# Optimization experiments

Measured on AMD Instinct MI355X. Metric: run time of the kernel, lower is better.

## Reference

```python
import jax, jax.numpy as jnp
import numpy as np

EPS = 1e-8  # torch F.cosine_similarity default eps


def setup_inputs() -> dict:
    key = jax.random.key(0)
    k1, k2 = jax.random.split(key)
    xs_pad = jax.random.normal(k1, (8, 4096, 512), dtype=jnp.float32)
    spk_emb = jax.random.normal(k2, (8, 256, 512), dtype=jnp.float32)
    return {"xs_pad": xs_pad, "spk_emb": spk_emb}


def reference(xs_pad, spk_emb):
    # Faithful to F.cosine_similarity(x.unsqueeze(2), y.unsqueeze(1), dim=-1):
    #   dot(x, y) / (max(||x||, eps) * max(||y||, eps))
    # Implemented as L2-normalize then a batched GEMM -> (B, T, S), avoiding
    # the (B, T, S, D) broadcast intermediate.
    x_norm = jnp.maximum(jnp.linalg.norm(xs_pad, axis=-1, keepdims=True), EPS)
    y_norm = jnp.maximum(jnp.linalg.norm(spk_emb, axis=-1, keepdims=True), EPS)
    xn = xs_pad / x_norm          # (B, T, D)
    yn = spk_emb / y_norm         # (B, S, D)
    scores = jnp.einsum('btd,bsd->bts', xn, yn)  # (B, T, S)
    return scores
```

## Files before the change

kernel.cpp:

```cpp
#include <hip/hip_runtime.h>
#include <hip/hip_bf16.h>

#define BB 8
#define TT 4096
#define SS 256
#define DD 512

typedef __attribute__((ext_vector_type(8))) short short8;
typedef __attribute__((ext_vector_type(4))) float floatx4;
typedef __attribute__((ext_vector_type(4))) int intx4;

__device__ inline int pk2(float a, float b) {
  __hip_bfloat162 h = __float22bfloat162_rn(make_float2(a, b));
  int r;
  __builtin_memcpy(&r, &h, 4);
  return r;
}

__device__ inline short8 cvt8(float4 f0, float4 f1) {
  intx4 p;
  p[0] = pk2(f0.x, f0.y);
  p[1] = pk2(f0.z, f0.w);
  p[2] = pk2(f1.x, f1.y);
  p[3] = pk2(f1.z, f1.w);
  return __builtin_bit_cast(short8, p);
}

__global__ __launch_bounds__(256) void cos_packB_kernel(
    const float* __restrict__ spk, short* __restrict__ bp) {
  const int id = blockIdx.x;
  const int ks = id & 1;
  const int kt = (id >> 1) & 7;
  const int wn = (id >> 4) & 1;
  const int tn = (id >> 5) & 1;
  const int b = id >> 6;
  const int t = threadIdx.x;
  const int in = t >> 6;
  const int lane = t & 63;
  const int row = tn * 128 + wn * 64 + in * 16 + (lane & 15);
  const int k = kt * 64 + ks * 32 + (lane >> 4) * 8;
  const float* src = spk + ((size_t)(b * SS + row)) * DD + k;
  float4 f0 = *(const float4*)src;
  float4 f1 = *(const float4*)(src + 4);
  short8 o = cvt8(f0, f1);
  size_t frag = (size_t)((((b * 2 + tn) * 2 + wn) * 8 + kt) * 2 + ks) * 4 + in;
  *(short8*)(bp + frag * 512 + (size_t)lane * 8) = o;
}

__global__ __launch_bounds__(256) void cos_fused_kernel(
    const float* __restrict__ xs, const short* __restrict__ bp,
    float* __restrict__ out) {
  __shared__ float sA[2 * 128 * 64];
  float* scX = sA;
  float* scY = sA + 128;

  const int tid = threadIdx.x;
  const int wave = tid >> 6;
  const int lane = tid & 63;

  const int id = blockIdx.x;
  const int xcd = id & 7;
  const int j = id >> 3;
  const int pairIdx = xcd * 32 + (j >> 1);
  const int tn = j & 1;
  const int tm = pairIdx & 31;
  const int b = pairIdx >> 5;

  const int wm = wave >> 1;
  const int wn = wave & 1;
  const int quad = lane >> 4;
  const int l15 = lane & 15;
  const bool gramA = (wm == wn);

  const float* Abase = xs + ((size_t)b * TT + tm * 128) * DD;
  const short* Bw =
      bp + (size_t)((b * 2 + tn) * 2 + wn) * 32768 + (size_t)lane * 8;

  floatx4 acc[4][4];
#pragma unroll
  for (int i = 0; i < 4; i++)
#pragma unroll
    for (int jj = 0; jj < 4; jj++) acc[i][jj] = (floatx4){0.f, 0.f, 0.f, 0.f};
  floatx4 accG[4];
#pragma unroll
  for (int i = 0; i < 4; i++) accG[i] = (floatx4){0.f, 0.f, 0.f, 0.f};

  int aoff[8];
#pragma unroll
  for (int jj = 0; jj < 8; jj++) {
    int s = jj * 256 + tid;
    int row = s >> 4;
    int blk = (s & 15) ^ (row & 15);
    aoff[jj] = row * DD + blk * 4;
  }

#pragma unroll
  for (int jj = 0; jj < 8; jj++) {
    __builtin_amdgcn_global_load_lds(
        (const __attribute__((address_space(1))) unsigned int*)(Abase +
            aoff[jj]),
        (__attribute__((address_space(3))) unsigned int*)(sA +
            (jj * 256 + wave * 64) * 4),
        16, 0, 0);
  }
  __syncthreads();

  for (int kt = 0; kt < 8; ++kt) {
    const int cur = kt & 1;

    short8 breg[2][4];
    const short* Bkt = Bw + kt * 4096;
#pragma unroll
    for (int ksl = 0; ksl < 2; ksl++)
#pragma unroll
      for (int in = 0; in < 4; in++)
        breg[ksl][in] = *(const short8*)(Bkt + ksl * 2048 + in * 512);

    if (kt < 7) {
#pragma unroll
      for (int jj = 0; jj < 8; jj++) {
        __builtin_amdgcn_global_load_lds(
            (const __attribute__((address_space(1))) unsigned int*)(Abase +
                aoff[jj] + (kt + 1) * 64),
            (__attribute__((address_space(3))) unsigned int*)(sA +
                (cur ^ 1) * 8192 + (jj * 256 + wave * 64) * 4),
            16, 0, 0);
      }
    }

    const float* sAc = sA + cur * 8192;
#pragma unroll
    for (int ks = 0; ks < 2; ks++) {
      short8 af[4];
      const int b0s = ks * 8 + quad * 2;
#pragma unroll
      for (int im = 0; im < 4; im++) {
        int row = wm * 64 + im * 16 + l15;
        int s0 = b0s ^ (row & 15);
        int s1 = (b0s + 1) ^ (row & 15);
        float4 f0 = *(const float4*)(sAc + row * 64 + s0 * 4);
        float4 f1 = *(const float4*)(sAc + row * 64 + s1 * 4);
        af[im] = cvt8(f0, f1);
      }
#pragma unroll
      for (int im = 0; im < 4; im++)
#pragma unroll
        for (int in = 0; in < 4; in++)
          acc[im][in] = __builtin_amdgcn_mfma_f32_16x16x32_bf16(
              af[im], breg[ks][in], acc[im][in], 0, 0, 0);
      if (gramA) {
#pragma unroll
        for (int im = 0; im < 4; im++)
          accG[im] = __builtin_amdgcn_mfma_f32_16x16x32_bf16(
              af[im], af[im], accG[im], 0, 0, 0);
      } else {
#pragma unroll
        for (int in = 0; in < 4; in++)
          accG[in] = __builtin_amdgcn_mfma_f32_16x16x32_bf16(
              breg[ks][in], breg[ks][in], accG[in], 0, 0, 0);
      }
    }
    __syncthreads();
  }

  if (quad == (l15 >> 2)) {
#pragma unroll
    for (int i = 0; i < 4; i++) {
      float inv = 1.0f / fmaxf(sqrtf(accG[i][l15 & 3]), 1e-8f);
      if (gramA)
        scX[wm * 64 + i * 16 + l15] = inv;
      else
        scY[wn * 64 + i * 16 + l15] = inv;
    }
  }
  __syncthreads();

  float* Obase = out + ((size_t)b * TT + tm * 128) * SS + tn * 128;
#pragma unroll
  for (int im = 0; im < 4; im++) {
#pragma unroll
    for (int in = 0; in < 4; in++) {
      int col = wn * 64 + in * 16 + l15;
      float yv = scY[col];
#pragma unroll
      for (int r = 0; r < 4; r++) {
        int row = wm * 64 + im * 16 + quad * 4 + r;
        Obase[row * SS + col] = acc[im][in][r] * scX[row] * yv;
      }
    }
  }
}

extern "C" void kernel_launch(void* const* d_in, const int* in_sizes, int n_in,
                              void* d_out, int out_size, void* d_ws,
                              size_t ws_size, hipStream_t stream) {
  const float* xs = (const float*)d_in[0];
  const float* spk = (const float*)d_in[1];
  float* out = (float*)d_out;
  short* bp = (short*)d_ws;

  hipLaunchKernelGGL(cos_packB_kernel, dim3(512), dim3(256), 0, stream, spk,
                     bp);
  hipLaunchKernelGGL(cos_fused_kernel, dim3(512), dim3(256), 0, stream, xs,
                     bp, out);
}
```

Baseline: 117.6 us.

## Deepen A-tile pipeline to four stages with half-width K slices and prefetched B

Replaces the two-buffer 64-wide K staging of the fp32 A tile with a four-buffer ring of 32-wide slices, keeping three tiles of global-to-LDS loads in flight. Explicit vmcnt waits and raw s_barrier replace the full __syncthreads, and B fragments are register-prefetched one step ahead. Launch bounds now request two blocks per CU. The aim is to hide global load latency behind MFMA work; in exchange the hand-tuned vmcnt counts are fragile, and the register cap may cause spills.

```diff
diff --git a/kernel.cpp b/kernel.cpp
--- a/kernel.cpp
+++ b/kernel.cpp
@@ -47,10 +47,10 @@
   *(short8*)(bp + frag * 512 + (size_t)lane * 8) = o;
 }
 
-__global__ __launch_bounds__(256) void cos_fused_kernel(
+__global__ __launch_bounds__(256, 2) void cos_fused_kernel(
     const float* __restrict__ xs, const short* __restrict__ bp,
     float* __restrict__ out) {
-  __shared__ float sA[2 * 128 * 64];
+  __shared__ float sA[4 * 128 * 32];
   float* scX = sA;
   float* scY = sA + 128;
 
@@ -85,83 +85,97 @@
 #pragma unroll
   for (int i = 0; i < 4; i++) accG[i] = (floatx4){0.f, 0.f, 0.f, 0.f};
 
-  int aoff[8];
-#pragma unroll
-  for (int jj = 0; jj < 8; jj++) {
+  int aoff[4];
+#pragma unroll
+  for (int jj = 0; jj < 4; jj++) {
     int s = jj * 256 + tid;
-    int row = s >> 4;
-    int blk = (s & 15) ^ (row & 15);
+    int row = s >> 3;
+    int blk = (s & 7) ^ (row & 7);
     aoff[jj] = row * DD + blk * 4;
   }
 
-#pragma unroll
-  for (int jj = 0; jj < 8; jj++) {
-    __builtin_amdgcn_global_load_lds(
-        (const __attribute__((address_space(1))) unsigned int*)(Abase +
-            aoff[jj]),
-        (__attribute__((address_space(3))) unsigned int*)(sA +
-            (jj * 256 + wave * 64) * 4),
-        16, 0, 0);
-  }
+#define STAGE(KT)                                                           \
+  do {                                                                      \
+    _Pragma("unroll") for (int jj = 0; jj < 4; jj++) {                      \
+      __builtin_amdgcn_global_load_lds(                                     \
+          (const __attribute__((address_space(1))) unsigned int*)(Abase +   \
+              aoff[jj] + (KT) * 32),                                        \
+          (__attribute__((address_space(3))) unsigned int*)(sA +            \
+              ((KT) & 3) * 4096 + (jj * 256 + wave * 64) * 4),              \
+          16, 0, 0);                                                        \
+    }                                                                       \
+  } while (0)
+
+  short8 breg[2][4];
+
+#pragma unroll
+  for (int in = 0; in < 4; in++)
+    breg[0][in] = *(const short8*)(Bw + in * 512);
+  STAGE(0);
+  __builtin_amdgcn_sched_barrier(0);
+  STAGE(1);
+  STAGE(2);
+  asm volatile("s_waitcnt vmcnt(8)" ::: "memory");
+  __builtin_amdgcn_sched_barrier(0);
+  __builtin_amdgcn_s_barrier();
+  __builtin_amdgcn_sched_barrier(0);
+
+#pragma unroll
+  for (int kt = 0; kt < 16; ++kt) {
+    if (kt + 1 < 16) {
+      const short* Bn = Bw + ((kt + 1) >> 1) * 4096 + ((kt + 1) & 1) * 2048;
+#pragma unroll
+      for (int in = 0; in < 4; in++)
+        breg[(kt + 1) & 1][in] = *(const short8*)(Bn + in * 512);
+    }
+    if (kt + 3 < 16) STAGE(kt + 3);
+
+    const float* sAc = sA + (kt & 3) * 4096;
+    short8 af[4];
+#pragma unroll
+    for (int im = 0; im < 4; im++) {
+      int row = wm * 64 + im * 16 + l15;
+      int r7 = l15 & 7;
+      int s0 = (quad * 2) ^ r7;
+      int s1 = (quad * 2 + 1) ^ r7;
+      float4 f0 = *(const float4*)(sAc + row * 32 + s0 * 4);
+      float4 f1 = *(const float4*)(sAc + row * 32 + s1 * 4);
+      af[im] = cvt8(f0, f1);
+    }
+#pragma unroll
+    for (int im = 0; im < 4; im++)
+#pragma unroll
+      for (int in = 0; in < 4; in++)
+        acc[im][in] = __builtin_amdgcn_mfma_f32_16x16x32_bf16(
+            af[im], breg[kt & 1][in], acc[im][in], 0, 0, 0);
+    if (gramA) {
+#pragma unroll
+      for (int im = 0; im < 4; im++)
+        accG[im] = __builtin_amdgcn_mfma_f32_16x16x32_bf16(
+            af[im], af[im], accG[im], 0, 0, 0);
+    } else {
+#pragma unroll
+      for (int in = 0; in < 4; in++)
+        accG[in] = __builtin_amdgcn_mfma_f32_16x16x32_bf16(
+            breg[kt & 1][in], breg[kt & 1][in], accG[in], 0, 0, 0);
+    }
+
+    if (kt < 15) {
+      if (kt == 0)
+        asm volatile("s_waitcnt vmcnt(12)" ::: "memory");
+      else if (kt <= 12)
+        asm volatile("s_waitcnt vmcnt(16)" ::: "memory");
+      else if (kt == 13)
+        asm volatile("s_waitcnt vmcnt(12)" ::: "memory");
+      else
+        asm volatile("s_waitcnt vmcnt(8)" ::: "memory");
+      __builtin_amdgcn_sched_barrier(0);
+      __builtin_amdgcn_s_barrier();
+      __builtin_amdgcn_sched_barrier(0);
+    }
+  }
+#undef STAGE
   __syncthreads();
-
-  for (int kt = 0; kt < 8; ++kt) {
-    const int cur = kt & 1;
-
-    short8 breg[2][4];
-    const short* Bkt = Bw + kt * 4096;
-#pragma unroll
-    for (int ksl = 0; ksl < 2; ksl++)
-#pragma unroll
-      for (int in = 0; in < 4; in++)
-        breg[ksl][in] = *(const short8*)(Bkt + ksl * 2048 + in * 512);
-
-    if (kt < 7) {
-#pragma unroll
-      for (int jj = 0; jj < 8; jj++) {
-        __builtin_amdgcn_global_load_lds(
-            (const __attribute__((address_space(1))) unsigned int*)(Abase +
-                aoff[jj] + (kt + 1) * 64),
-            (__attribute__((address_space(3))) unsigned int*)(sA +
-                (cur ^ 1) * 8192 + (jj * 256 + wave * 64) * 4),
-            16, 0, 0);
-      }
-    }
-
-    const float* sAc = sA + cur * 8192;
-#pragma unroll
-    for (int ks = 0; ks < 2; ks++) {
-      short8 af[4];
-      const int b0s = ks * 8 + quad * 2;
-#pragma unroll
-      for (int im = 0; im < 4; im++) {
-        int row = wm * 64 + im * 16 + l15;
-        int s0 = b0s ^ (row & 15);
-        int s1 = (b0s + 1) ^ (row & 15);
-        float4 f0 = *(const float4*)(sAc + row * 64 + s0 * 4);
-        float4 f1 = *(const float4*)(sAc + row * 64 + s1 * 4);
-        af[im] = cvt8(f0, f1);
-      }
-#pragma unroll
-      for (int im = 0; im < 4; im++)
-#pragma unroll
-        for (int in = 0; in < 4; in++)
-          acc[im][in] = __builtin_amdgcn_mfma_f32_16x16x32_bf16(
-              af[im], breg[ks][in], acc[im][in], 0, 0, 0);
-      if (gramA) {
-#pragma unroll
-        for (int im = 0; im < 4; im++)
-          accG[im] = __builtin_amdgcn_mfma_f32_16x16x32_bf16(
-              af[im], af[im], accG[im], 0, 0, 0);
-      } else {
-#pragma unroll
-        for (int in = 0; in < 4; in++)
-          accG[in] = __builtin_amdgcn_mfma_f32_16x16x32_bf16(
-              breg[ks][in], breg[ks][in], accG[in], 0, 0, 0);
-      }
-    }
-    __syncthreads();
-  }
 
   if (quad == (l15 >> 2)) {
 #pragma unroll
```

New measurement: 120.1 us. 1.02x slower.

## Load A fragments directly from global into registers with 3-stage prefetch

Applied to the files above, without the earlier changes.

Replaces the LDS-staged A tile (global_load_lds with double buffering and per-k-tile barriers) with direct per-lane global float4 loads into a triple-buffered register pipeline, prefetching two k-slices ahead together with B fragments. This removes LDS traffic and the __syncthreads in the main loop, and lowers LDS use so more blocks can be resident. In exchange, each wave pair with the same wm now loads its A rows separately, doubling A global/L2 traffic, and the register buffers raise VGPR pressure, which could lower occupancy.

```diff
diff --git a/kernel.cpp b/kernel.cpp
--- a/kernel.cpp
+++ b/kernel.cpp
@@ -50,9 +50,8 @@
 __global__ __launch_bounds__(256) void cos_fused_kernel(
     const float* __restrict__ xs, const short* __restrict__ bp,
     float* __restrict__ out) {
-  __shared__ float sA[2 * 128 * 64];
-  float* scX = sA;
-  float* scY = sA + 128;
+  __shared__ float scX[128];
+  __shared__ float scY[128];
 
   const int tid = threadIdx.x;
   const int wave = tid >> 6;
@@ -72,7 +71,13 @@
   const int l15 = lane & 15;
   const bool gramA = (wm == wn);
 
-  const float* Abase = xs + ((size_t)b * TT + tm * 128) * DD;
+  const float* Arow[4];
+#pragma unroll
+  for (int im = 0; im < 4; im++)
+    Arow[im] = xs +
+               ((size_t)b * TT + tm * 128 + wm * 64 + im * 16 + l15) * DD +
+               quad * 8;
+
   const short* Bw =
       bp + (size_t)((b * 2 + tn) * 2 + wn) * 32768 + (size_t)lane * 8;
 
@@ -85,83 +90,62 @@
 #pragma unroll
   for (int i = 0; i < 4; i++) accG[i] = (floatx4){0.f, 0.f, 0.f, 0.f};
 
-  int aoff[8];
-#pragma unroll
-  for (int jj = 0; jj < 8; jj++) {
-    int s = jj * 256 + tid;
-    int row = s >> 4;
-    int blk = (s & 15) ^ (row & 15);
-    aoff[jj] = row * DD + blk * 4;
-  }
+  float4 abuf[3][8];
+  short8 bbuf[3][4];
+
+#define LOADA(S)                                                        \
+  do {                                                                  \
+    _Pragma("unroll") for (int im_ = 0; im_ < 4; im_++) {               \
+      const float* p_ = Arow[im_] + ((S) >> 1) * 64 + ((S) & 1) * 32;   \
+      abuf[(S) % 3][im_ * 2] = *(const float4*)p_;                      \
+      abuf[(S) % 3][im_ * 2 + 1] = *(const float4*)(p_ + 4);            \
+    }                                                                   \
+  } while (0)
+
+#define LOADB(S)                                                        \
+  do {                                                                  \
+    const short* q_ = Bw + ((S) >> 1) * 4096 + ((S) & 1) * 2048;        \
+    _Pragma("unroll") for (int in_ = 0; in_ < 4; in_++)                 \
+      bbuf[(S) % 3][in_] = *(const short8*)(q_ + in_ * 512);            \
+  } while (0)
+
+  LOADA(0);
+  LOADB(0);
+  LOADA(1);
+  LOADB(1);
 
 #pragma unroll
-  for (int jj = 0; jj < 8; jj++) {
-    __builtin_amdgcn_global_load_lds(
-        (const __attribute__((address_space(1))) unsigned int*)(Abase +
-            aoff[jj]),
-        (__attribute__((address_space(3))) unsigned int*)(sA +
-            (jj * 256 + wave * 64) * 4),
-        16, 0, 0);
-  }
-  __syncthreads();
+  for (int s = 0; s < 16; ++s) {
+    if (s + 2 < 16) {
+      LOADA(s + 2);
+      LOADB(s + 2);
+    }
 
-  for (int kt = 0; kt < 8; ++kt) {
-    const int cur = kt & 1;
+    short8 af[4];
+#pragma unroll
+    for (int im = 0; im < 4; im++)
+      af[im] = cvt8(abuf[s % 3][im * 2], abuf[s % 3][im * 2 + 1]);
 
-    short8 breg[2][4];
-    const short* Bkt = Bw + kt * 4096;
 #pragma unroll
-    for (int ksl = 0; ksl < 2; ksl++)
+    for (int im = 0; im < 4; im++)
 #pragma unroll
       for (int in = 0; in < 4; in++)
-        breg[ksl][in] = *(const short8*)(Bkt + ksl * 2048 + in * 512);
-
-    if (kt < 7) {
-#pragma unroll
-      for (int jj = 0; jj < 8; jj++) {
-        __builtin_amdgcn_global_load_lds(
-            (const __attribute__((address_space(1))) unsigned int*)(Abase +
-                aoff[jj] + (kt + 1) * 64),
-            (__attribute__((address_space(3))) unsigned int*)(sA +
-                (cur ^ 1) * 8192 + (jj * 256 + wave * 64) * 4),
-            16, 0, 0);
-      }
-    }
-
-    const float* sAc = sA + cur * 8192;
-#pragma unroll
-    for (int ks = 0; ks < 2; ks++) {
-      short8 af[4];
-      const int b0s = ks * 8 + quad * 2;
-#pragma unroll
-      for (int im = 0; im < 4; im++) {
-        int row = wm * 64 + im * 16 + l15;
-        int s0 = b0s ^ (row & 15);
-        int s1 = (b0s + 1) ^ (row & 15);
-        float4 f0 = *(const float4*)(sAc + row * 64 + s0 * 4);
-        float4 f1 = *(const float4*)(sAc + row * 64 + s1 * 4);
-        af[im] = cvt8(f0, f1);
-      }
+        acc[im][in] = __builtin_amdgcn_mfma_f32_16x16x32_bf16(
+            af[im], bbuf[s % 3][in], acc[im][in], 0, 0, 0);
+    if (gramA) {
 #pragma unroll
       for (int im = 0; im < 4; im++)
+        accG[im] = __builtin_amdgcn_mfma_f32_16x16x32_bf16(
+            af[im], af[im], accG[im], 0, 0, 0);
+    } else {
 #pragma unroll
-        for (int in = 0; in < 4; in++)
-          acc[im][in] = __builtin_amdgcn_mfma_f32_16x16x32_bf16(
-              af[im], breg[ks][in], acc[im][in], 0, 0, 0);
-      if (gramA) {
-#pragma unroll
-        for (int im = 0; im < 4; im++)
-          accG[im] = __builtin_amdgcn_mfma_f32_16x16x32_bf16(
-              af[im], af[im], accG[im], 0, 0, 0);
-      } else {
-#pragma unroll
-        for (int in = 0; in < 4; in++)
-          accG[in] = __builtin_amdgcn_mfma_f32_16x16x32_bf16(
-              breg[ks][in], breg[ks][in], accG[in], 0, 0, 0);
-      }
+      for (int in = 0; in < 4; in++)
+        accG[in] = __builtin_amdgcn_mfma_f32_16x16x32_bf16(
+            bbuf[s % 3][in], bbuf[s % 3][in], accG[in], 0, 0, 0);
     }
-    __syncthreads();
   }
+#undef LOADA
+#undef LOADB
 
   if (quad == (l15 >> 2)) {
 #pragma unroll
```

After: 127.3 us. 1.08x slower.
